# Kernel tuning notes

Hardware: AMD Instinct MI355X
Metric: run time of the kernel (lower is better)

The kernel has to match this reference:

```python
import jax, jax.numpy as jnp
import numpy as np

N_NODES = 50000; N_EDGES = 600000; N_GRAPHS = 128
IN_CH = 128; PROJ = 128; OUT_CH = 128; K = 3; NCLASS = 2; EPS = 1e-5


def _mask():
    # xhi_layer_mask: block i (rows i*OUT_CH:(i+1)*OUT_CH) sees first PROJ*(i+1) input cols
    blocks = []
    for i in range(K):
        m = np.zeros((OUT_CH, PROJ * K), np.float32)
        m[:, :PROJ * (i + 1)] = 1.0
        blocks.append(m)
    return jnp.asarray(np.concatenate(blocks, 0))


def _bn(x, g, b):
    # BatchNorm1d in training mode: biased batch stats, affine g/b
    m = jnp.mean(x, axis=0)
    v = jnp.var(x, axis=0)
    return (x - m) * jax.lax.rsqrt(v + EPS) * g + b


def setup_inputs() -> dict:
    key = jax.random.key(0)
    ks = jax.random.split(key, 10)
    M = OUT_CH * K
    def w(k, shape):
        return jax.random.normal(k, shape, jnp.float32) * 0.05
    return {
        "x": jax.random.normal(ks[0], (N_NODES, IN_CH), jnp.float32),
        "edge_index": jax.random.randint(ks[1], (2, N_EDGES), 0, N_NODES),
        "batch": jnp.sort(jax.random.randint(ks[2], (N_NODES,), 0, N_GRAPHS)),
        "n_graphs": N_GRAPHS,
        "w_rel": w(ks[3], (PROJ, IN_CH)), "b_rel": jnp.zeros((PROJ,), jnp.float32),
        "w_root": w(ks[4], (PROJ, IN_CH)),
        "norm0_g": jnp.ones((PROJ,), jnp.float32), "norm0_b": jnp.zeros((PROJ,), jnp.float32),
        "lin_w": w(ks[5], (M, PROJ * K)), "lin_b": jnp.zeros((M,), jnp.float32),
        "bnh_g": jnp.ones((M,), jnp.float32), "bnh_b": jnp.zeros((M,), jnp.float32),
        "bno_g": jnp.ones((3 * M,), jnp.float32), "bno_b": jnp.zeros((3 * M,), jnp.float32),
        "w1": w(ks[6], (2 * M, 3 * M)), "b1": jnp.zeros((2 * M,), jnp.float32),
        "w2": w(ks[7], (M, 2 * M)), "b2": jnp.zeros((M,), jnp.float32),
        "w3": w(ks[8], (NCLASS, M)), "b3": jnp.zeros((NCLASS,), jnp.float32),
    }


def reference(x, edge_index, batch, n_graphs, w_rel, b_rel, w_root, norm0_g, norm0_b,
              lin_w, lin_b, bnh_g, bnh_b, bno_g, bno_b, w1, b1, w2, b2, w3, b3):
    row, col = edge_index[0], edge_index[1]
    # GraphConv: lin_rel(sum_{j->i} x_j) + lin_root(x_i)
    neigh = jax.ops.segment_sum(x[row], col, num_segments=N_NODES)
    X = neigh @ w_rel.T + b_rel + x @ w_root.T
    X = _bn(X, norm0_g, norm0_b)
    # k-hop polynomial diffusion: A^i X computed as iterative SpMM over edges
    # (A[r,c] = 1 for edge (r,c): (A v)[r] = sum over edges of v[c])
    H = [X]
    cur = X
    for _ in range(K - 1):
        cur = jax.ops.segment_sum(cur[col], row, num_segments=N_NODES)
        H.append(cur)
    Hc = jnp.concatenate(H, axis=1)  # [N, PROJ*K]
    Hm = _bn(Hc @ (lin_w * _mask()).T + lin_b, bnh_g, bnh_b)  # [N, OUT_CH*K]
    # global mean / add / max pooling per graph
    ones = jnp.ones((N_NODES,), jnp.float32)
    cnt = jax.ops.segment_sum(ones, batch, num_segments=n_graphs)
    Hadd = jax.ops.segment_sum(Hm, batch, num_segments=n_graphs)
    Havg = Hadd / jnp.maximum(cnt, 1.0)[:, None]
    Hmax = jax.ops.segment_max(Hm, batch, num_segments=n_graphs)
    Hmax = jnp.where(jnp.isfinite(Hmax), Hmax, 0.0)  # guard empty segments
    Hcat = jnp.concatenate([Havg, Hadd, Hmax], axis=1)  # [G, 3*OUT_CH*K]
    # funnel readout (dropout = identity in eval)
    h = _bn(Hcat, bno_g, bno_b)
    h = jax.nn.relu(h @ w1.T + b1)
    h = jax.nn.relu(h @ w2.T + b2)
    return jax.nn.log_softmax(h @ w3.T + b3, axis=1)
```

## Files before the change

kernel.cpp:

```cpp
#include <hip/hip_runtime.h>
#include <math.h>

#define N_NODES 50000
#define N_EDGES 600000
#define N_GRAPHS 128
#define IN_CH 128
#define PROJ 128
#define OUT_CH 128
#define M_DIM 384
#define HC_DIM 384
#define CAT_DIM 1152
#define H1_DIM 768
#define EPS 1e-5f
#define SCAN_BLK 256
#define NPART 8
#define PART_NODES 6250
#define NPB 64
#define NROWB 391

using bf16x8 = __attribute__((ext_vector_type(8))) short;
using f32x4  = __attribute__((ext_vector_type(4))) float;

__device__ inline unsigned short f2bf(float f) {
  unsigned u = __float_as_uint(f);
  unsigned r = u + 0x7fffu + ((u >> 16) & 1u);
  return (unsigned short)(r >> 16);
}
__device__ inline float bf2f(unsigned h) {
  return __uint_as_float(h << 16);
}

__device__ inline void atomicMaxF(float* addr, float val) {
  int iv = __float_as_int(val);
  if (iv >= 0) atomicMax((int*)addr, iv);
  else         atomicMin((unsigned int*)addr, (unsigned int)iv);
}
__device__ inline void atomicMinF(float* addr, float val) {
  int iv = __float_as_int(val);
  if (iv >= 0) atomicMin((int*)addr, iv);
  else         atomicMax((unsigned int*)addr, (unsigned int)iv);
}

__device__ inline void gld16(const void* g, void* l) {
  __builtin_amdgcn_global_load_lds(
      (const __attribute__((address_space(1))) void*)g,
      (__attribute__((address_space(3))) void*)l, 16, 0, 0);
}

__global__ void init_kernel(const int* __restrict__ batch, float* __restrict__ gmax,
                            float* __restrict__ gmin, int* __restrict__ start) {
  int i = blockIdx.x * blockDim.x + threadIdx.x;
  if (i < N_GRAPHS * M_DIM) {
    gmax[i] = -__builtin_inff();
    gmin[i] =  __builtin_inff();
  }
  if (i < N_NODES) {
    int b = batch[i];
    int bp = (i == 0) ? -1 : batch[i - 1];
    for (int g = bp + 1; g <= b; ++g) start[g] = i;
    if (i == N_NODES - 1)
      for (int g = b + 1; g <= N_GRAPHS; ++g) start[g] = N_NODES;
  }
}

__global__ void cnt_from_bounds_kernel(const int* __restrict__ start, float* __restrict__ cnt) {
  int g = threadIdx.x;
  if (g < N_GRAPHS) cnt[g] = (float)(start[g + 1] - start[g]);
}

__global__ __launch_bounds__(256) void hist_part_kernel(
    const int* __restrict__ row, const int* __restrict__ col,
    int* __restrict__ degA, int* __restrict__ degB) {
  const int part = blockIdx.x & (NPART - 1);
  const int slice = blockIdx.x >> 3;
  const int lo = part * PART_NODES, hi = lo + PART_NODES;
  for (int e = slice * 256 + threadIdx.x; e < N_EDGES; e += NPB * 256) {
    int r = row[e], c = col[e];
    if (c >= lo && c < hi) atomicAdd(&degA[c], 1);
    if (r >= lo && r < hi) atomicAdd(&degB[r], 1);
  }
}

__global__ __launch_bounds__(256) void fill_csr_part_kernel(
    const int* __restrict__ row, const int* __restrict__ col,
    int* __restrict__ cursA, int* __restrict__ eidxA,
    int* __restrict__ cursB, int* __restrict__ eidxB) {
  const int part = blockIdx.x & (NPART - 1);
  const int slice = blockIdx.x >> 3;
  const int lo = part * PART_NODES, hi = lo + PART_NODES;
  for (int e = slice * 256 + threadIdx.x; e < N_EDGES; e += NPB * 256) {
    int r = row[e], c = col[e];
    if (c >= lo && c < hi) eidxA[atomicAdd(&cursA[c], 1)] = r;
    if (r >= lo && r < hi) eidxB[atomicAdd(&cursB[r], 1)] = c;
  }
}

__global__ void scan1_kernel(const int* __restrict__ degA, const int* __restrict__ degB,
                             int* __restrict__ offsA, int* __restrict__ offsB,
                             int* __restrict__ bsumA, int* __restrict__ bsumB, int n) {
  __shared__ int sh[SCAN_BLK];
  const int* deg = blockIdx.y ? degB : degA;
  int* offs = blockIdx.y ? offsB : offsA;
  int* bsum = blockIdx.y ? bsumB : bsumA;
  int i = blockIdx.x * SCAN_BLK + threadIdx.x;
  int v = (i < n) ? deg[i] : 0;
  sh[threadIdx.x] = v; __syncthreads();
  #pragma unroll
  for (int d = 1; d < SCAN_BLK; d <<= 1) {
    int t = (threadIdx.x >= d) ? sh[threadIdx.x - d] : 0;
    __syncthreads();
    sh[threadIdx.x] += t;
    __syncthreads();
  }
  if (i < n) offs[i] = sh[threadIdx.x] - v;
  if (threadIdx.x == SCAN_BLK - 1) bsum[blockIdx.x] = sh[threadIdx.x];
}

__global__ void scan2_kernel(int* __restrict__ bsumA, int* __restrict__ bsumB, int nb) {
  __shared__ int sh[SCAN_BLK];
  int* bsum = blockIdx.y ? bsumB : bsumA;
  int v = (threadIdx.x < nb) ? bsum[threadIdx.x] : 0;
  sh[threadIdx.x] = v; __syncthreads();
  #pragma unroll
  for (int d = 1; d < SCAN_BLK; d <<= 1) {
    int t = (threadIdx.x >= d) ? sh[threadIdx.x - d] : 0;
    __syncthreads();
    sh[threadIdx.x] += t;
    __syncthreads();
  }
  if (threadIdx.x < nb) bsum[threadIdx.x] = sh[threadIdx.x] - v;
}

__global__ void scan3_kernel(int* __restrict__ offsA, int* __restrict__ offsB,
                             const int* __restrict__ bsumA, const int* __restrict__ bsumB,
                             int* __restrict__ cursA, int* __restrict__ cursB, int n) {
  int* offs = blockIdx.y ? offsB : offsA;
  const int* bsum = blockIdx.y ? bsumB : bsumA;
  int* cursor = blockIdx.y ? cursB : cursA;
  int i = blockIdx.x * SCAN_BLK + threadIdx.x;
  if (i < n) {
    int o = offs[i] + bsum[blockIdx.x];
    offs[i] = o;
    cursor[i] = o;
  }
}

__global__ void convert_x_kernel(const float* __restrict__ x, unsigned short* __restrict__ xnb) {
  int t = blockIdx.x * blockDim.x + threadIdx.x;
  if (t >= N_NODES * 32) return;
  int node = t >> 5;
  int c4 = (t & 31) << 2;
  float4 v = *(const float4*)(x + (size_t)node * IN_CH + c4);
  ushort4 h = {f2bf(v.x), f2bf(v.y), f2bf(v.z), f2bf(v.w)};
  *(ushort4*)(xnb + (size_t)node * 256 + 128 + c4) = h;
}

__global__ void convert_wcat_kernel(const float* __restrict__ w_rel, const float* __restrict__ w_root,
                                    unsigned short* __restrict__ wcatb) {
  int t = blockIdx.x * blockDim.x + threadIdx.x;
  if (t >= 128 * 64) return;
  int n = t >> 6;
  int c4 = (t & 63) << 2;
  const float* src = (c4 < 128) ? (w_rel + (size_t)n * 128 + c4)
                                : (w_root + (size_t)n * 128 + (c4 - 128));
  float4 v = *(const float4*)src;
  ushort4 h = {f2bf(v.x), f2bf(v.y), f2bf(v.z), f2bf(v.w)};
  *(ushort4*)(wcatb + (size_t)n * 256 + c4) = h;
}

__global__ void convert_linw_kernel(const float* __restrict__ lin_w, unsigned short* __restrict__ linwb) {
  int t = blockIdx.x * blockDim.x + threadIdx.x;
  if (t >= 384 * 96) return;
  int n = t / 96;
  int c4 = (t - n * 96) << 2;
  float4 v = *(const float4*)(lin_w + (size_t)n * HC_DIM + c4);
  ushort4 h = {f2bf(v.x), f2bf(v.y), f2bf(v.z), f2bf(v.w)};
  *(ushort4*)(linwb + (size_t)n * HC_DIM + c4) = h;
}

__device__ inline void addbf8(float* a, uint4 v) {
  a[0] += bf2f(v.x & 0xffffu); a[1] += bf2f(v.x >> 16);
  a[2] += bf2f(v.y & 0xffffu); a[3] += bf2f(v.y >> 16);
  a[4] += bf2f(v.z & 0xffffu); a[5] += bf2f(v.z >> 16);
  a[6] += bf2f(v.w & 0xffffu); a[7] += bf2f(v.w >> 16);
}

__global__ __launch_bounds__(256) void gather_bf16_kernel(
    const unsigned short* __restrict__ src, const int* __restrict__ offs,
    const int* __restrict__ ends, const int* __restrict__ eidx,
    unsigned short* __restrict__ dst, int src_ld, int dst_ld) {
  int tid = blockIdx.x * blockDim.x + threadIdx.x;
  int node = tid >> 4;
  int c = (tid & 15) << 3;
  if (node >= N_NODES) return;
  int j = offs[node], end = ends[node];
  float a[8] = {0.f, 0.f, 0.f, 0.f, 0.f, 0.f, 0.f, 0.f};
  for (; j + 3 < end; j += 4) {
    int s0 = eidx[j], s1 = eidx[j + 1], s2 = eidx[j + 2], s3 = eidx[j + 3];
    uint4 v0 = *(const uint4*)(src + (size_t)s0 * src_ld + c);
    uint4 v1 = *(const uint4*)(src + (size_t)s1 * src_ld + c);
    uint4 v2 = *(const uint4*)(src + (size_t)s2 * src_ld + c);
    uint4 v3 = *(const uint4*)(src + (size_t)s3 * src_ld + c);
    addbf8(a, v0); addbf8(a, v1); addbf8(a, v2); addbf8(a, v3);
  }
  for (; j < end; ++j) {
    uint4 v0 = *(const uint4*)(src + (size_t)eidx[j] * src_ld + c);
    addbf8(a, v0);
  }
  uint4 o;
  o.x = (unsigned)f2bf(a[0]) | ((unsigned)f2bf(a[1]) << 16);
  o.y = (unsigned)f2bf(a[2]) | ((unsigned)f2bf(a[3]) << 16);
  o.z = (unsigned)f2bf(a[4]) | ((unsigned)f2bf(a[5]) << 16);
  o.w = (unsigned)f2bf(a[6]) | ((unsigned)f2bf(a[7]) << 16);
  *(uint4*)(dst + (size_t)node * dst_ld + c) = o;
}

__device__ inline void stage_async(const unsigned short* __restrict__ src, int src_ld,
                                   int row0, int k0, char* __restrict__ zone, int t) {
  #pragma unroll
  for (int p = 0; p < 4; ++p) {
    int idx = p * 256 + t;
    int r = idx >> 3;
    int slot = idx & 7;
    int sslot = slot ^ (r & 7);
    const char* g = (const char*)(src + (size_t)(row0 + r) * src_ld + k0) + (sslot << 4);
    void* l = zone + p * 4096 + (t >> 6) * 1024;
    gld16(g, l);
  }
}

__device__ inline bf16x8 frag_ld(const char* __restrict__ zone, int row, int slot) {
  return *(const bf16x8*)(zone + row * 128 + ((slot ^ (row & 7)) << 4));
}

__global__ __launch_bounds__(256) void gemm_conv_mfma(
    const unsigned short* __restrict__ xnb, const unsigned short* __restrict__ wcatb,
    const float* __restrict__ b_rel, float* __restrict__ Hc0,
    float* __restrict__ colsum8, float* __restrict__ colsq8) {
  __shared__ char smem[32768];
  char* zoneA = smem;
  char* zoneB = smem + 16384;
  const int bm = blockIdx.x * 128;
  const int t = threadIdx.x;
  const int l = t & 63;
  const int wid = t >> 6;
  const int wr = wid >> 1, wc = wid & 1;
  const int lrow = l & 15, lk = l >> 4;
  f32x4 acc[4][4];
  #pragma unroll
  for (int i = 0; i < 4; ++i)
    #pragma unroll
    for (int jn = 0; jn < 4; ++jn) acc[i][jn] = (f32x4){0.f, 0.f, 0.f, 0.f};
  for (int st = 0; st < 4; ++st) {
    __syncthreads();
    stage_async(xnb, 256, bm, st * 64, zoneA, t);
    stage_async(wcatb, 256, 0, st * 64, zoneB, t);
    __syncthreads();
    #pragma unroll
    for (int kk = 0; kk < 2; ++kk) {
      bf16x8 af[4], bfr[4];
      #pragma unroll
      for (int mf = 0; mf < 4; ++mf) af[mf] = frag_ld(zoneA, wr * 64 + mf * 16 + lrow, kk * 4 + lk);
      #pragma unroll
      for (int nf = 0; nf < 4; ++nf) bfr[nf] = frag_ld(zoneB, wc * 64 + nf * 16 + lrow, kk * 4 + lk);
      #pragma unroll
      for (int mf = 0; mf < 4; ++mf)
        #pragma unroll
        for (int nf = 0; nf < 4; ++nf)
          acc[mf][nf] = __builtin_amdgcn_mfma_f32_16x16x32_bf16(af[mf], bfr[nf], acc[mf][nf], 0, 0, 0);
    }
  }
  float brv[4];
  #pragma unroll
  for (int nf = 0; nf < 4; ++nf) brv[nf] = b_rel[wc * 64 + nf * 16 + lrow];
  #pragma unroll
  for (int mf = 0; mf < 4; ++mf) {
    #pragma unroll
    for (int q = 0; q < 4; ++q) {
      int r = bm + wr * 64 + mf * 16 + lk * 4 + q;
      if (r < N_NODES) {
        #pragma unroll
        for (int nf = 0; nf < 4; ++nf)
          Hc0[(size_t)r * 128 + wc * 64 + nf * 16 + lrow] = acc[mf][nf][q] + brv[nf];
      }
    }
  }
  __syncthreads();
  float* csum = (float*)smem;
  float* csq  = (float*)(smem + 512);
  if (t < 128) { csum[t] = 0.f; csq[t] = 0.f; }
  __syncthreads();
  #pragma unroll
  for (int nf = 0; nf < 4; ++nf) {
    int ccol = wc * 64 + nf * 16 + lrow;
    float s = 0.f, q = 0.f;
    #pragma unroll
    for (int mf = 0; mf < 4; ++mf)
      #pragma unroll
      for (int qq = 0; qq < 4; ++qq) {
        int r = bm + wr * 64 + mf * 16 + lk * 4 + qq;
        if (r < N_NODES) { float v = acc[mf][nf][qq] + brv[nf]; s += v; q += v * v; }
      }
    atomicAdd(&csum[ccol], s);
    atomicAdd(&csq[ccol], q);
  }
  __syncthreads();
  if (t < 128) {
    int cpy = (blockIdx.x & 7) * 128;
    atomicAdd(&colsum8[cpy + t], csum[t]);
    atomicAdd(&colsq8[cpy + t], csq[t]);
  }
}

__global__ void bn_prep_kernel(const float* __restrict__ colsum8, const float* __restrict__ colsq8,
                               const float* __restrict__ g_, const float* __restrict__ b_,
                               float* __restrict__ bn_s, float* __restrict__ bn_t) {
  int c = threadIdx.x;
  float s1 = 0.f, s2 = 0.f;
  #pragma unroll
  for (int k = 0; k < 8; ++k) { s1 += colsum8[k * 128 + c]; s2 += colsq8[k * 128 + c]; }
  float m = s1 * (1.0f / N_NODES);
  float var = s2 * (1.0f / N_NODES) - m * m;
  float sc = g_[c] * rsqrtf(var + EPS);
  bn_s[c] = sc;
  bn_t[c] = b_[c] - m * sc;
}

__global__ __launch_bounds__(256) void gemm_mask_mfma(
    const unsigned short* __restrict__ Hcb, const unsigned short* __restrict__ linwb,
    const float* __restrict__ lin_b, const int* __restrict__ batch,
    float* __restrict__ gsum, float* __restrict__ gmax, float* __restrict__ gmin,
    float* __restrict__ colsumsq) {
  __shared__ char smem[33792];
  __shared__ int bsh[128];
  char* zoneA = smem;
  char* zoneB = smem + 16384;
  const int bid = blockIdx.x;
  const int ybl = 2 - bid / NROWB;
  const int bm = (bid % NROWB) * 128;
  const int bn = ybl * 128;
  const int nstages = 2 * (ybl + 1);
  const int t = threadIdx.x;
  const int l = t & 63;
  const int wid = t >> 6;
  const int wr = wid >> 1, wc = wid & 1;
  const int lrow = l & 15, lk = l >> 4;
  f32x4 acc[4][4];
  #pragma unroll
  for (int i = 0; i < 4; ++i)
    #pragma unroll
    for (int jn = 0; jn < 4; ++jn) acc[i][jn] = (f32x4){0.f, 0.f, 0.f, 0.f};
  for (int st = 0; st < nstages; ++st) {
    __syncthreads();
    stage_async(Hcb, HC_DIM, bm, st * 64, zoneA, t);
    stage_async(linwb, HC_DIM, bn, st * 64, zoneB, t);
    __syncthreads();
    #pragma unroll
    for (int kk = 0; kk < 2; ++kk) {
      bf16x8 af[4], bfr[4];
      #pragma unroll
      for (int mf = 0; mf < 4; ++mf) af[mf] = frag_ld(zoneA, wr * 64 + mf * 16 + lrow, kk * 4 + lk);
      #pragma unroll
      for (int nf = 0; nf < 4; ++nf) bfr[nf] = frag_ld(zoneB, wc * 64 + nf * 16 + lrow, kk * 4 + lk);
      #pragma unroll
      for (int mf = 0; mf < 4; ++mf)
        #pragma unroll
        for (int nf = 0; nf < 4; ++nf)
          acc[mf][nf] = __builtin_amdgcn_mfma_f32_16x16x32_bf16(af[mf], bfr[nf], acc[mf][nf], 0, 0, 0);
    }
  }
  float lbv[4];
  #pragma unroll
  for (int nf = 0; nf < 4; ++nf) lbv[nf] = lin_b[bn + wc * 64 + nf * 16 + lrow];
  if (t < 128) bsh[t] = (bm + t < N_NODES) ? batch[bm + t] : -1;
  float* Y = (float*)smem;
  const int col = t & 127;
  const int gcol = bn + col;
  const int r0 = (t >> 7) * 32;
  float sq = 0.f;
  __syncthreads();
  for (int half = 0; half < 2; ++half) {
    if (wr == half) {
      #pragma unroll
      for (int mf = 0; mf < 4; ++mf)
        #pragma unroll
        for (int q = 0; q < 4; ++q) {
          int rr = mf * 16 + lk * 4 + q;
          #pragma unroll
          for (int nf = 0; nf < 4; ++nf)
            Y[rr * 132 + wc * 64 + nf * 16 + lrow] = acc[mf][nf][q] + lbv[nf];
        }
    }
    __syncthreads();
    int curg = -1;
    float s = 0.f, mx = 0.f, mn = 0.f;
    for (int rr = 0; rr < 32; ++rr) {
      int g = bsh[half * 64 + r0 + rr];
      if (g < 0) break;
      float y = Y[(r0 + rr) * 132 + col];
      sq += y * y;
      if (g != curg) {
        if (curg >= 0) {
          atomicAdd(&gsum[curg * M_DIM + gcol], s);
          atomicMaxF(&gmax[curg * M_DIM + gcol], mx);
          atomicMinF(&gmin[curg * M_DIM + gcol], mn);
        }
        curg = g; s = y; mx = y; mn = y;
      } else {
        s += y; mx = fmaxf(mx, y); mn = fminf(mn, y);
      }
    }
    if (curg >= 0) {
      atomicAdd(&gsum[curg * M_DIM + gcol], s);
      atomicMaxF(&gmax[curg * M_DIM + gcol], mx);
      atomicMinF(&gmin[curg * M_DIM + gcol], mn);
    }
    __syncthreads();
  }
  atomicAdd(&colsumsq[gcol], sq);
}

__global__ __launch_bounds__(256) void bn_apply0_kernel(
    const float* __restrict__ Hc0, unsigned short* __restrict__ Hcb,
    const float* __restrict__ bn_s, const float* __restrict__ bn_t) {
  int tid = blockIdx.x * blockDim.x + threadIdx.x;
  if (tid >= N_NODES * 32) return;
  int r = tid >> 5;
  int c = (tid & 31) << 2;
  float4 v = *(const float4*)(Hc0 + (size_t)r * 128 + c);
  float vv[4] = {v.x, v.y, v.z, v.w};
  #pragma unroll
  for (int j = 0; j < 4; ++j)
    vv[j] = vv[j] * bn_s[c + j] + bn_t[c + j];
  ushort4 hh = {f2bf(vv[0]), f2bf(vv[1]), f2bf(vv[2]), f2bf(vv[3])};
  *(ushort4*)(Hcb + (size_t)r * HC_DIM + c) = hh;
}

__device__ inline float block_sum128(float v, float* red) {
  int t = threadIdx.x;
  red[t] = v; __syncthreads();
  #pragma unroll
  for (int s = 64; s >= 1; s >>= 1) {
    if (t < s) red[t] += red[t + s];
    __syncthreads();
  }
  float r = red[0];
  __syncthreads();
  return r;
}

__device__ inline void bn_write_col(float v, int col, const float* __restrict__ bg,
                                    const float* __restrict__ bb, float* __restrict__ h0T,
                                    float* red) {
  float s1 = block_sum128(v, red);
  float s2 = block_sum128(v * v, red);
  float m = s1 * (1.0f / N_GRAPHS);
  float var = s2 * (1.0f / N_GRAPHS) - m * m;
  float sc = bg[col] * rsqrtf(var + EPS);
  h0T[(size_t)col * N_GRAPHS + threadIdx.x] = (v - m) * sc + bb[col];
}

__global__ __launch_bounds__(128) void finalize_kernel(
    const float* __restrict__ gsum, const float* __restrict__ gmax,
    const float* __restrict__ gmin, const float* __restrict__ colsumsq,
    const float* __restrict__ cnt, const float* __restrict__ bnh_g,
    const float* __restrict__ bnh_b, const float* __restrict__ bno_g,
    const float* __restrict__ bno_b, float* __restrict__ h0T) {
  __shared__ float red[128];
  int c = blockIdx.x;
  int g = threadIdx.x;
  float vsum = gsum[g * M_DIM + c];
  float colsum = block_sum128(vsum, red);
  float m = colsum * (1.0f / N_NODES);
  float var = colsumsq[c] * (1.0f / N_NODES) - m * m;
  float s = bnh_g[c] * rsqrtf(var + EPS);
  float t = bnh_b[c] - m * s;
  float cg = cnt[g];
  float hadd = s * vsum + cg * t;
  float havg = hadd / fmaxf(cg, 1.0f);
  float hmax = 0.f;
  if (cg > 0.f)
    hmax = (s >= 0.f ? s * gmax[g * M_DIM + c] : s * gmin[g * M_DIM + c]) + t;
  bn_write_col(havg, c,        bno_g, bno_b, h0T, red);
  bn_write_col(hadd, 384 + c,  bno_g, bno_b, h0T, red);
  bn_write_col(hmax, 768 + c,  bno_g, bno_b, h0T, red);
}

__global__ __launch_bounds__(128) void mlp_kernel(
    const float* __restrict__ inT, const float* __restrict__ W,
    const float* __restrict__ bias, float* __restrict__ outT, int Kdim, int do_relu) {
  __shared__ float wrow[CAT_DIM];
  int oc = blockIdx.x;
  int g = threadIdx.x;
  for (int k = g; k < Kdim; k += 128) wrow[k] = W[(size_t)oc * Kdim + k];
  __syncthreads();
  float acc = bias[oc];
  for (int k = 0; k < Kdim; ++k) acc += inT[(size_t)k * N_GRAPHS + g] * wrow[k];
  if (do_relu) acc = fmaxf(acc, 0.f);
  outT[(size_t)oc * N_GRAPHS + g] = acc;
}

__global__ __launch_bounds__(128) void head_kernel(
    const float* __restrict__ h2T, const float* __restrict__ w3,
    const float* __restrict__ b3, float* __restrict__ out) {
  int g = threadIdx.x;
  float z0 = b3[0], z1 = b3[1];
  for (int k = 0; k < M_DIM; ++k) {
    float v = h2T[(size_t)k * N_GRAPHS + g];
    z0 += v * w3[k];
    z1 += v * w3[M_DIM + k];
  }
  float mz = fmaxf(z0, z1);
  float lse = mz + logf(expf(z0 - mz) + expf(z1 - mz));
  out[g * 2 + 0] = z0 - lse;
  out[g * 2 + 1] = z1 - lse;
}

extern "C" void kernel_launch(void* const* d_in, const int* in_sizes, int n_in,
                              void* d_out, int out_size, void* d_ws, size_t ws_size,
                              hipStream_t stream) {
  const float* x       = (const float*)d_in[0];
  const int*   row     = (const int*)d_in[1];
  const int*   col     = row + N_EDGES;
  const int*   batch   = (const int*)d_in[2];
  const float* w_rel   = (const float*)d_in[4];
  const float* b_rel   = (const float*)d_in[5];
  const float* w_root  = (const float*)d_in[6];
  const float* norm0_g = (const float*)d_in[7];
  const float* norm0_b = (const float*)d_in[8];
  const float* lin_w   = (const float*)d_in[9];
  const float* lin_b   = (const float*)d_in[10];
  const float* bnh_g   = (const float*)d_in[11];
  const float* bnh_b   = (const float*)d_in[12];
  const float* bno_g   = (const float*)d_in[13];
  const float* bno_b   = (const float*)d_in[14];
  const float* w1      = (const float*)d_in[15];
  const float* b1      = (const float*)d_in[16];
  const float* w2      = (const float*)d_in[17];
  const float* b2      = (const float*)d_in[18];
  const float* w3      = (const float*)d_in[19];
  const float* b3      = (const float*)d_in[20];
  float* out = (float*)d_out;

  char* ws = (char*)d_ws;
  size_t off = 0;
  auto allocb = [&](size_t nbytes) {
    char* p = ws + off;
    off += ((nbytes + 255) & ~(size_t)255);
    return p;
  };
  int*   degA      = (int*)allocb(N_NODES * 4);
  int*   degB      = (int*)allocb(N_NODES * 4);
  float* gsum      = (float*)allocb((size_t)N_GRAPHS * M_DIM * 4);
  float* colsumsq  = (float*)allocb(M_DIM * 4);
  float* colsum8   = (float*)allocb(8 * PROJ * 4);
  float* colsq8    = (float*)allocb(8 * PROJ * 4);
  size_t zero_bytes = off;
  float* cnt    = (float*)allocb(N_GRAPHS * 4);
  int*   gstart = (int*)allocb((N_GRAPHS + 1) * 4);
  float* bn_s   = (float*)allocb(PROJ * 4);
  float* bn_t   = (float*)allocb(PROJ * 4);
  int*   offsA = (int*)allocb(N_NODES * 4);
  int*   cursA = (int*)allocb(N_NODES * 4);
  int*   offsB = (int*)allocb(N_NODES * 4);
  int*   cursB = (int*)allocb(N_NODES * 4);
  int*   bsumA = (int*)allocb(SCAN_BLK * 4);
  int*   bsumB = (int*)allocb(SCAN_BLK * 4);
  int*   eidxA = (int*)allocb(N_EDGES * 4);
  int*   eidxB = (int*)allocb(N_EDGES * 4);
  float* Hc0   = (float*)allocb((size_t)N_NODES * 128 * 4);
  unsigned short* Hcb   = (unsigned short*)allocb((size_t)N_NODES * HC_DIM * 2);
  unsigned short* xnb   = (unsigned short*)allocb((size_t)N_NODES * 256 * 2);
  unsigned short* wcatb = (unsigned short*)allocb(128 * 256 * 2);
  unsigned short* linwb = (unsigned short*)allocb(384 * 384 * 2);
  float* gmax  = (float*)allocb((size_t)N_GRAPHS * M_DIM * 4);
  float* gmin  = (float*)allocb((size_t)N_GRAPHS * M_DIM * 4);
  float* h0T   = (float*)allocb((size_t)CAT_DIM * N_GRAPHS * 4);
  float* h1T   = (float*)allocb((size_t)H1_DIM * N_GRAPHS * 4);
  float* h2T   = (float*)allocb((size_t)M_DIM * N_GRAPHS * 4);

  const int NB = (N_NODES + SCAN_BLK - 1) / SCAN_BLK;

  hipMemsetAsync(d_ws, 0, zero_bytes, stream);
  init_kernel<<<(N_NODES + 255) / 256, 256, 0, stream>>>(batch, gmax, gmin, gstart);
  cnt_from_bounds_kernel<<<1, 128, 0, stream>>>(gstart, cnt);

  hist_part_kernel<<<NPART * NPB, 256, 0, stream>>>(row, col, degA, degB);
  scan1_kernel<<<dim3(NB, 2), SCAN_BLK, 0, stream>>>(degA, degB, offsA, offsB, bsumA, bsumB, N_NODES);
  scan2_kernel<<<dim3(1, 2), SCAN_BLK, 0, stream>>>(bsumA, bsumB, NB);
  scan3_kernel<<<dim3(NB, 2), SCAN_BLK, 0, stream>>>(offsA, offsB, bsumA, bsumB, cursA, cursB, N_NODES);
  fill_csr_part_kernel<<<NPART * NPB, 256, 0, stream>>>(row, col, cursA, eidxA, cursB, eidxB);

  convert_x_kernel<<<(N_NODES * 32 + 255) / 256, 256, 0, stream>>>(x, xnb);
  convert_wcat_kernel<<<(128 * 64 + 255) / 256, 256, 0, stream>>>(w_rel, w_root, wcatb);
  convert_linw_kernel<<<(384 * 96 + 255) / 256, 256, 0, stream>>>(lin_w, linwb);

  gather_bf16_kernel<<<(N_NODES * 16 + 255) / 256, 256, 0, stream>>>(
      xnb + 128, offsA, cursA, eidxA, xnb, 256, 256);
  gemm_conv_mfma<<<NROWB, 256, 0, stream>>>(xnb, wcatb, b_rel, Hc0, colsum8, colsq8);
  bn_prep_kernel<<<1, 128, 0, stream>>>(colsum8, colsq8, norm0_g, norm0_b, bn_s, bn_t);
  bn_apply0_kernel<<<(N_NODES * 32 + 255) / 256, 256, 0, stream>>>(Hc0, Hcb, bn_s, bn_t);
  gather_bf16_kernel<<<(N_NODES * 16 + 255) / 256, 256, 0, stream>>>(
      Hcb, offsB, cursB, eidxB, Hcb + 128, HC_DIM, HC_DIM);
  gather_bf16_kernel<<<(N_NODES * 16 + 255) / 256, 256, 0, stream>>>(
      Hcb + 128, offsB, cursB, eidxB, Hcb + 256, HC_DIM, HC_DIM);
  gemm_mask_mfma<<<NROWB * 3, 256, 0, stream>>>(
      Hcb, linwb, lin_b, batch, gsum, gmax, gmin, colsumsq);
  finalize_kernel<<<M_DIM, 128, 0, stream>>>(gsum, gmax, gmin, colsumsq, cnt,
                                             bnh_g, bnh_b, bno_g, bno_b, h0T);
  mlp_kernel<<<H1_DIM, 128, 0, stream>>>(h0T, w1, b1, h1T, CAT_DIM, 1);
  mlp_kernel<<<M_DIM, 128, 0, stream>>>(h1T, w2, b2, h2T, H1_DIM, 1);
  head_kernel<<<1, 128, 0, stream>>>(h2T, w3, b3, out);
}
```

Measured before the change: 394.8 us.

## Fold first BatchNorm into lin weights and gather, double-buffer GEMM staging

The first BatchNorm's affine transform is now applied algebraically. Its scale is folded into the first 128 columns of lin_w, and its shift goes into a new bias lin_b2. The first diffusion gather applies scale*sum + deg*shift to the raw conv output, which lets the separate bn_apply pass and the fp32 Hc0 buffer be dropped: gemm_conv now writes bf16 directly into Hcb. Both MFMA GEMMs also switch to double-buffered LDS staging, using 64KB of shared memory, so the next K-slice loads while the current one computes. The risks are lower occupancy from the larger LDS footprint and changed bf16 rounding, since the pre-BN values are now stored in bf16.

```diff
diff --git a/kernel.cpp b/kernel.cpp
--- a/kernel.cpp
+++ b/kernel.cpp
@@ -168,14 +168,27 @@
   *(ushort4*)(wcatb + (size_t)n * 256 + c4) = h;
 }
 
-__global__ void convert_linw_kernel(const float* __restrict__ lin_w, unsigned short* __restrict__ linwb) {
+__global__ void convert_linw_kernel(const float* __restrict__ lin_w, const float* __restrict__ bn_s,
+                                    unsigned short* __restrict__ linwb) {
   int t = blockIdx.x * blockDim.x + threadIdx.x;
   if (t >= 384 * 96) return;
   int n = t / 96;
   int c4 = (t - n * 96) << 2;
   float4 v = *(const float4*)(lin_w + (size_t)n * HC_DIM + c4);
+  if (c4 < 128) {
+    v.x *= bn_s[c4 + 0]; v.y *= bn_s[c4 + 1]; v.z *= bn_s[c4 + 2]; v.w *= bn_s[c4 + 3];
+  }
   ushort4 h = {f2bf(v.x), f2bf(v.y), f2bf(v.z), f2bf(v.w)};
   *(ushort4*)(linwb + (size_t)n * HC_DIM + c4) = h;
+}
+
+__global__ void linb_fold_kernel(const float* __restrict__ lin_w, const float* __restrict__ lin_b,
+                                 const float* __restrict__ bn_t, float* __restrict__ lin_b2) {
+  int o = blockIdx.x * blockDim.x + threadIdx.x;
+  if (o >= M_DIM) return;
+  float s = lin_b[o];
+  for (int c = 0; c < 128; ++c) s += bn_t[c] * lin_w[(size_t)o * HC_DIM + c];
+  lin_b2[o] = s;
 }
 
 __device__ inline void addbf8(float* a, uint4 v) {
@@ -183,6 +196,32 @@
   a[2] += bf2f(v.y & 0xffffu); a[3] += bf2f(v.y >> 16);
   a[4] += bf2f(v.z & 0xffffu); a[5] += bf2f(v.z >> 16);
   a[6] += bf2f(v.w & 0xffffu); a[7] += bf2f(v.w >> 16);
+}
+
+__device__ inline void gather_body(const unsigned short* __restrict__ src,
+                                   const int* __restrict__ eidx, int j, int end,
+                                   int src_ld, int c, float* a) {
+  for (; j + 3 < end; j += 4) {
+    int s0 = eidx[j], s1 = eidx[j + 1], s2 = eidx[j + 2], s3 = eidx[j + 3];
+    uint4 v0 = *(const uint4*)(src + (size_t)s0 * src_ld + c);
+    uint4 v1 = *(const uint4*)(src + (size_t)s1 * src_ld + c);
+    uint4 v2 = *(const uint4*)(src + (size_t)s2 * src_ld + c);
+    uint4 v3 = *(const uint4*)(src + (size_t)s3 * src_ld + c);
+    addbf8(a, v0); addbf8(a, v1); addbf8(a, v2); addbf8(a, v3);
+  }
+  for (; j < end; ++j) {
+    uint4 v0 = *(const uint4*)(src + (size_t)eidx[j] * src_ld + c);
+    addbf8(a, v0);
+  }
+}
+
+__device__ inline void store_bf8(unsigned short* dst, const float* a) {
+  uint4 o;
+  o.x = (unsigned)f2bf(a[0]) | ((unsigned)f2bf(a[1]) << 16);
+  o.y = (unsigned)f2bf(a[2]) | ((unsigned)f2bf(a[3]) << 16);
+  o.z = (unsigned)f2bf(a[4]) | ((unsigned)f2bf(a[5]) << 16);
+  o.w = (unsigned)f2bf(a[6]) | ((unsigned)f2bf(a[7]) << 16);
+  *(uint4*)dst = o;
 }
 
 __global__ __launch_bounds__(256) void gather_bf16_kernel(
@@ -193,26 +232,27 @@
   int node = tid >> 4;
   int c = (tid & 15) << 3;
   if (node >= N_NODES) return;
-  int j = offs[node], end = ends[node];
   float a[8] = {0.f, 0.f, 0.f, 0.f, 0.f, 0.f, 0.f, 0.f};
-  for (; j + 3 < end; j += 4) {
-    int s0 = eidx[j], s1 = eidx[j + 1], s2 = eidx[j + 2], s3 = eidx[j + 3];
-    uint4 v0 = *(const uint4*)(src + (size_t)s0 * src_ld + c);
-    uint4 v1 = *(const uint4*)(src + (size_t)s1 * src_ld + c);
-    uint4 v2 = *(const uint4*)(src + (size_t)s2 * src_ld + c);
-    uint4 v3 = *(const uint4*)(src + (size_t)s3 * src_ld + c);
-    addbf8(a, v0); addbf8(a, v1); addbf8(a, v2); addbf8(a, v3);
-  }
-  for (; j < end; ++j) {
-    uint4 v0 = *(const uint4*)(src + (size_t)eidx[j] * src_ld + c);
-    addbf8(a, v0);
-  }
-  uint4 o;
-  o.x = (unsigned)f2bf(a[0]) | ((unsigned)f2bf(a[1]) << 16);
-  o.y = (unsigned)f2bf(a[2]) | ((unsigned)f2bf(a[3]) << 16);
-  o.z = (unsigned)f2bf(a[4]) | ((unsigned)f2bf(a[5]) << 16);
-  o.w = (unsigned)f2bf(a[6]) | ((unsigned)f2bf(a[7]) << 16);
-  *(uint4*)(dst + (size_t)node * dst_ld + c) = o;
+  gather_body(src, eidx, offs[node], ends[node], src_ld, c, a);
+  store_bf8(dst + (size_t)node * dst_ld + c, a);
+}
+
+__global__ __launch_bounds__(256) void gather_bn_kernel(
+    const unsigned short* __restrict__ src, const int* __restrict__ offs,
+    const int* __restrict__ ends, const int* __restrict__ eidx,
+    const float* __restrict__ bn_s, const float* __restrict__ bn_t,
+    unsigned short* __restrict__ dst, int src_ld, int dst_ld) {
+  int tid = blockIdx.x * blockDim.x + threadIdx.x;
+  int node = tid >> 4;
+  int c = (tid & 15) << 3;
+  if (node >= N_NODES) return;
+  int j0 = offs[node], end = ends[node];
+  float a[8] = {0.f, 0.f, 0.f, 0.f, 0.f, 0.f, 0.f, 0.f};
+  gather_body(src, eidx, j0, end, src_ld, c, a);
+  float deg = (float)(end - j0);
+  #pragma unroll
+  for (int k = 0; k < 8; ++k) a[k] = bn_s[c + k] * a[k] + deg * bn_t[c + k];
+  store_bf8(dst + (size_t)node * dst_ld + c, a);
 }
 
 __device__ inline void stage_async(const unsigned short* __restrict__ src, int src_ld,
@@ -235,11 +275,9 @@
 
 __global__ __launch_bounds__(256) void gemm_conv_mfma(
     const unsigned short* __restrict__ xnb, const unsigned short* __restrict__ wcatb,
-    const float* __restrict__ b_rel, float* __restrict__ Hc0,
+    const float* __restrict__ b_rel, unsigned short* __restrict__ Hcb,
     float* __restrict__ colsum8, float* __restrict__ colsq8) {
-  __shared__ char smem[32768];
-  char* zoneA = smem;
-  char* zoneB = smem + 16384;
+  __shared__ char smem[65536];
   const int bm = blockIdx.x * 128;
   const int t = threadIdx.x;
   const int l = t & 63;
@@ -251,24 +289,33 @@
   for (int i = 0; i < 4; ++i)
     #pragma unroll
     for (int jn = 0; jn < 4; ++jn) acc[i][jn] = (f32x4){0.f, 0.f, 0.f, 0.f};
+  stage_async(xnb, 256, bm, 0, smem, t);
+  stage_async(wcatb, 256, 0, 0, smem + 16384, t);
+  __syncthreads();
+  int cur = 0;
   for (int st = 0; st < 4; ++st) {
-    __syncthreads();
-    stage_async(xnb, 256, bm, st * 64, zoneA, t);
-    stage_async(wcatb, 256, 0, st * 64, zoneB, t);
-    __syncthreads();
+    if (st < 3) {
+      char* nz = smem + (cur ^ 1) * 32768;
+      stage_async(xnb, 256, bm, (st + 1) * 64, nz, t);
+      stage_async(wcatb, 256, 0, (st + 1) * 64, nz + 16384, t);
+    }
+    const char* zA = smem + cur * 32768;
+    const char* zB = zA + 16384;
     #pragma unroll
     for (int kk = 0; kk < 2; ++kk) {
       bf16x8 af[4], bfr[4];
       #pragma unroll
-      for (int mf = 0; mf < 4; ++mf) af[mf] = frag_ld(zoneA, wr * 64 + mf * 16 + lrow, kk * 4 + lk);
-      #pragma unroll
-      for (int nf = 0; nf < 4; ++nf) bfr[nf] = frag_ld(zoneB, wc * 64 + nf * 16 + lrow, kk * 4 + lk);
+      for (int mf = 0; mf < 4; ++mf) af[mf] = frag_ld(zA, wr * 64 + mf * 16 + lrow, kk * 4 + lk);
+      #pragma unroll
+      for (int nf = 0; nf < 4; ++nf) bfr[nf] = frag_ld(zB, wc * 64 + nf * 16 + lrow, kk * 4 + lk);
       #pragma unroll
       for (int mf = 0; mf < 4; ++mf)
         #pragma unroll
         for (int nf = 0; nf < 4; ++nf)
           acc[mf][nf] = __builtin_amdgcn_mfma_f32_16x16x32_bf16(af[mf], bfr[nf], acc[mf][nf], 0, 0, 0);
     }
+    __syncthreads();
+    cur ^= 1;
   }
   float brv[4];
   #pragma unroll
@@ -281,7 +328,7 @@
       if (r < N_NODES) {
         #pragma unroll
         for (int nf = 0; nf < 4; ++nf)
-          Hc0[(size_t)r * 128 + wc * 64 + nf * 16 + lrow] = acc[mf][nf][q] + brv[nf];
+          Hcb[(size_t)r * HC_DIM + wc * 64 + nf * 16 + lrow] = f2bf(acc[mf][nf][q] + brv[nf]);
       }
     }
   }
@@ -328,13 +375,11 @@
 
 __global__ __launch_bounds__(256) void gemm_mask_mfma(
     const unsigned short* __restrict__ Hcb, const unsigned short* __restrict__ linwb,
-    const float* __restrict__ lin_b, const int* __restrict__ batch,
+    const float* __restrict__ lin_b2, const int* __restrict__ batch,
     float* __restrict__ gsum, float* __restrict__ gmax, float* __restrict__ gmin,
     float* __restrict__ colsumsq) {
-  __shared__ char smem[33792];
+  __shared__ char smem[65536];
   __shared__ int bsh[128];
-  char* zoneA = smem;
-  char* zoneB = smem + 16384;
   const int bid = blockIdx.x;
   const int ybl = 2 - bid / NROWB;
   const int bm = (bid % NROWB) * 128;
@@ -350,28 +395,37 @@
   for (int i = 0; i < 4; ++i)
     #pragma unroll
     for (int jn = 0; jn < 4; ++jn) acc[i][jn] = (f32x4){0.f, 0.f, 0.f, 0.f};
+  stage_async(Hcb, HC_DIM, bm, 0, smem, t);
+  stage_async(linwb, HC_DIM, bn, 0, smem + 16384, t);
+  __syncthreads();
+  int cur = 0;
   for (int st = 0; st < nstages; ++st) {
-    __syncthreads();
-    stage_async(Hcb, HC_DIM, bm, st * 64, zoneA, t);
-    stage_async(linwb, HC_DIM, bn, st * 64, zoneB, t);
-    __syncthreads();
+    if (st + 1 < nstages) {
+      char* nz = smem + (cur ^ 1) * 32768;
+      stage_async(Hcb, HC_DIM, bm, (st + 1) * 64, nz, t);
+      stage_async(linwb, HC_DIM, bn, (st + 1) * 64, nz + 16384, t);
+    }
+    const char* zA = smem + cur * 32768;
+    const char* zB = zA + 16384;
     #pragma unroll
     for (int kk = 0; kk < 2; ++kk) {
       bf16x8 af[4], bfr[4];
       #pragma unroll
-      for (int mf = 0; mf < 4; ++mf) af[mf] = frag_ld(zoneA, wr * 64 + mf * 16 + lrow, kk * 4 + lk);
-      #pragma unroll
-      for (int nf = 0; nf < 4; ++nf) bfr[nf] = frag_ld(zoneB, wc * 64 + nf * 16 + lrow, kk * 4 + lk);
+      for (int mf = 0; mf < 4; ++mf) af[mf] = frag_ld(zA, wr * 64 + mf * 16 + lrow, kk * 4 + lk);
+      #pragma unroll
+      for (int nf = 0; nf < 4; ++nf) bfr[nf] = frag_ld(zB, wc * 64 + nf * 16 + lrow, kk * 4 + lk);
       #pragma unroll
       for (int mf = 0; mf < 4; ++mf)
         #pragma unroll
         for (int nf = 0; nf < 4; ++nf)
           acc[mf][nf] = __builtin_amdgcn_mfma_f32_16x16x32_bf16(af[mf], bfr[nf], acc[mf][nf], 0, 0, 0);
     }
+    __syncthreads();
+    cur ^= 1;
   }
   float lbv[4];
   #pragma unroll
-  for (int nf = 0; nf < 4; ++nf) lbv[nf] = lin_b[bn + wc * 64 + nf * 16 + lrow];
+  for (int nf = 0; nf < 4; ++nf) lbv[nf] = lin_b2[bn + wc * 64 + nf * 16 + lrow];
   if (t < 128) bsh[t] = (bm + t < N_NODES) ? batch[bm + t] : -1;
   float* Y = (float*)smem;
   const int col = t & 127;
@@ -418,22 +472,6 @@
     __syncthreads();
   }
   atomicAdd(&colsumsq[gcol], sq);
-}
-
-__global__ __launch_bounds__(256) void bn_apply0_kernel(
-    const float* __restrict__ Hc0, unsigned short* __restrict__ Hcb,
-    const float* __restrict__ bn_s, const float* __restrict__ bn_t) {
-  int tid = blockIdx.x * blockDim.x + threadIdx.x;
-  if (tid >= N_NODES * 32) return;
-  int r = tid >> 5;
-  int c = (tid & 31) << 2;
-  float4 v = *(const float4*)(Hc0 + (size_t)r * 128 + c);
-  float vv[4] = {v.x, v.y, v.z, v.w};
-  #pragma unroll
-  for (int j = 0; j < 4; ++j)
-    vv[j] = vv[j] * bn_s[c + j] + bn_t[c + j];
-  ushort4 hh = {f2bf(vv[0]), f2bf(vv[1]), f2bf(vv[2]), f2bf(vv[3])};
-  *(ushort4*)(Hcb + (size_t)r * HC_DIM + c) = hh;
 }
 
 __device__ inline float block_sum128(float v, float* red) {
@@ -560,6 +598,7 @@
   int*   gstart = (int*)allocb((N_GRAPHS + 1) * 4);
   float* bn_s   = (float*)allocb(PROJ * 4);
   float* bn_t   = (float*)allocb(PROJ * 4);
+  float* lin_b2 = (float*)allocb(M_DIM * 4);
   int*   offsA = (int*)allocb(N_NODES * 4);
   int*   cursA = (int*)allocb(N_NODES * 4);
   int*   offsB = (int*)allocb(N_NODES * 4);
@@ -568,7 +607,6 @@
   int*   bsumB = (int*)allocb(SCAN_BLK * 4);
   int*   eidxA = (int*)allocb(N_EDGES * 4);
   int*   eidxB = (int*)allocb(N_EDGES * 4);
-  float* Hc0   = (float*)allocb((size_t)N_NODES * 128 * 4);
   unsigned short* Hcb   = (unsigned short*)allocb((size_t)N_NODES * HC_DIM * 2);
   unsigned short* xnb   = (unsigned short*)allocb((size_t)N_NODES * 256 * 2);
   unsigned short* wcatb = (unsigned short*)allocb(128 * 256 * 2);
@@ -593,19 +631,19 @@
 
   convert_x_kernel<<<(N_NODES * 32 + 255) / 256, 256, 0, stream>>>(x, xnb);
   convert_wcat_kernel<<<(128 * 64 + 255) / 256, 256, 0, stream>>>(w_rel, w_root, wcatb);
-  convert_linw_kernel<<<(384 * 96 + 255) / 256, 256, 0, stream>>>(lin_w, linwb);
 
   gather_bf16_kernel<<<(N_NODES * 16 + 255) / 256, 256, 0, stream>>>(
       xnb + 128, offsA, cursA, eidxA, xnb, 256, 256);
-  gemm_conv_mfma<<<NROWB, 256, 0, stream>>>(xnb, wcatb, b_rel, Hc0, colsum8, colsq8);
+  gemm_conv_mfma<<<NROWB, 256, 0, stream>>>(xnb, wcatb, b_rel, Hcb, colsum8, colsq8);
   bn_prep_kernel<<<1, 128, 0, stream>>>(colsum8, colsq8, norm0_g, norm0_b, bn_s, bn_t);
-  bn_apply0_kernel<<<(N_NODES * 32 + 255) / 256, 256, 0, stream>>>(Hc0, Hcb, bn_s, bn_t);
-  gather_bf16_kernel<<<(N_NODES * 16 + 255) / 256, 256, 0, stream>>>(
-      Hcb, offsB, cursB, eidxB, Hcb + 128, HC_DIM, HC_DIM);
+  convert_linw_kernel<<<(384 * 96 + 255) / 256, 256, 0, stream>>>(lin_w, bn_s, linwb);
+  linb_fold_kernel<<<3, 128, 0, stream>>>(lin_w, lin_b, bn_t, lin_b2);
+  gather_bn_kernel<<<(N_NODES * 16 + 255) / 256, 256, 0, stream>>>(
+      Hcb, offsB, cursB, eidxB, bn_s, bn_t, Hcb + 128, HC_DIM, HC_DIM);
   gather_bf16_kernel<<<(N_NODES * 16 + 255) / 256, 256, 0, stream>>>(
       Hcb + 128, offsB, cursB, eidxB, Hcb + 256, HC_DIM, HC_DIM);
   gemm_mask_mfma<<<NROWB * 3, 256, 0, stream>>>(
-      Hcb, linwb, lin_b, batch, gsum, gmax, gmin, colsumsq);
+      Hcb, linwb, lin_b2, batch, gsum, gmax, gmin, colsumsq);
   finalize_kernel<<<M_DIM, 128, 0, stream>>>(gsum, gmax, gmin, colsumsq, cnt,
                                              bnh_g, bnh_b, bno_g, bno_b, h0T);
   mlp_kernel<<<H1_DIM, 128, 0, stream>>>(h0T, w1, b1, h1T, CAT_DIM, 1);
```

Measured after the change: 400.0 us. About the same (+1.3%).
